# Optimization experiments

Hardware: AMD Instinct MI355X
Metric: run time of the kernel (lower is better)

Reference implementation:

```python
import jax, jax.numpy as jnp
import numpy as np

S, B, D, H = 2048, 64, 128, 128


def setup_inputs() -> dict:
    key = jax.random.key(0)
    ks = jax.random.split(key, 7)
    scale = 1.0 / np.sqrt(H)
    return {
        "input": jax.random.normal(ks[0], (S, B, D), dtype=jnp.float32),
        "time": jax.random.uniform(ks[1], (S, B, 1), dtype=jnp.float32),
        "W_ih": jax.random.normal(ks[2], (4 * H, D), dtype=jnp.float32) * scale,
        "W_hh": jax.random.normal(ks[3], (4 * H, H), dtype=jnp.float32) * scale,
        "b": jax.random.normal(ks[4], (4 * H,), dtype=jnp.float32) * scale,
        "w_t": jax.random.uniform(ks[5], (H,), dtype=jnp.float32),
        "b_t": jax.random.uniform(ks[6], (H,), dtype=jnp.float32),
    }


def reference(input, time, W_ih, W_hh, b, w_t, b_t):
    # ReverseLSTMLayer: run a time-conditioned LSTM cell over REVERSED time steps,
    # then re-reverse the stacked outputs. state starts at zeros (state=None).
    Bsz = input.shape[1]
    Hd = W_hh.shape[1]

    def step(state, xt):
        x, t = xt  # x: [B, D], t: [B, 1]
        h, c = state
        gates = x @ W_ih.T + h @ W_hh.T + b  # [B, 4H]
        i_, f_, g_, o_ = jnp.split(gates, 4, axis=-1)
        i_ = jax.nn.sigmoid(i_)
        f_ = jax.nn.sigmoid(f_)
        g_ = jnp.tanh(g_)
        o_ = jax.nn.sigmoid(o_)
        # learned exponential time decay on the carried cell state (T-LSTM style)
        decay = jnp.exp(-jax.nn.relu(t * w_t + b_t))  # [B, H]
        c = f_ * c * decay + i_ * g_
        h = o_ * jnp.tanh(c)
        return (h, c), h

    init = (jnp.zeros((Bsz, Hd), input.dtype), jnp.zeros((Bsz, Hd), input.dtype))
    # iterate over reversed sequence, then reverse outputs back
    (h, c), ys_rev = jax.lax.scan(step, init, (input[::-1], time[::-1]))
    outputs = ys_rev[::-1]  # [S, B, H]
    return outputs, (h, c)
```

## Files before the change

kernel.cpp:

```cpp
#include <hip/hip_runtime.h>

#define S_LEN 2048
#define B_SZ  64
#define D_IN  128
#define H_SZ  128
#define G4    512

typedef __attribute__((ext_vector_type(4))) float     floatx4;
typedef __attribute__((ext_vector_type(2))) float     floatx2;
typedef __attribute__((ext_vector_type(8))) _Float16  half8;
typedef __attribute__((ext_vector_type(2))) _Float16  half2_t;

template<int CTRL>
__device__ __forceinline__ float qperm(float v) {
  return __int_as_float(
      __builtin_amdgcn_mov_dpp(__float_as_int(v), CTRL, 0xF, 0xF, true));
}

template<int P>
__device__ __forceinline__ half2_t h2ext(half8 v) {
  return __builtin_shufflevector(v, v, 2 * P, 2 * P + 1);
}

__device__ __forceinline__ void lds_barrier() {
  asm volatile("s_waitcnt lgkmcnt(0)\n\ts_barrier" ::: "memory");
}

__global__ __launch_bounds__(256) void gx_gemm(
    const float* __restrict__ X,
    const float* __restrict__ Wih,
    const float* __restrict__ bias,
    _Float16* __restrict__ gx)
{
  __shared__ _Float16 Wl[128][136];
  const int tid  = threadIdx.x;
  const int lane = tid & 63;
  const int wv   = tid >> 6;
  const int R0   = blockIdx.x * 256;
  const int m    = lane & 15;
  const int q    = lane >> 4;

  const float LOG2E = 1.4426950408889634f;

  half8 afrag[4][4];
  #pragma unroll
  for (int rg = 0; rg < 4; ++rg) {
    const float* xrow = X + (size_t)(R0 + rg * 64 + wv * 16 + m) * D_IN;
    #pragma unroll
    for (int kf = 0; kf < 4; ++kf) {
      const int k0 = kf * 32 + q * 8;
      floatx4 v0 = *(const floatx4*)(xrow + k0);
      floatx4 v1 = *(const floatx4*)(xrow + k0 + 4);
      half8 a;
      a[0] = (_Float16)v0.x; a[1] = (_Float16)v0.y;
      a[2] = (_Float16)v0.z; a[3] = (_Float16)v0.w;
      a[4] = (_Float16)v1.x; a[5] = (_Float16)v1.y;
      a[6] = (_Float16)v1.z; a[7] = (_Float16)v1.w;
      afrag[rg][kf] = a;
    }
  }

  for (int nc = 0; nc < 4; ++nc) {
    const float sc = (nc == 2) ? (-2.0f * LOG2E) : (-LOG2E);
    __syncthreads();
    for (int i = tid; i < 128 * 32; i += 256) {
      const int row = i >> 5;
      const int c4  = (i & 31) * 4;
      floatx4 v = *(const floatx4*)(Wih + ((size_t)nc * 128 + row) * D_IN + c4);
      Wl[row][c4 + 0] = (_Float16)v.x;
      Wl[row][c4 + 1] = (_Float16)v.y;
      Wl[row][c4 + 2] = (_Float16)v.z;
      Wl[row][c4 + 3] = (_Float16)v.w;
    }
    __syncthreads();

    #pragma unroll
    for (int nt = 0; nt < 8; ++nt) {
      const int n0  = nc * 128 + nt * 16;
      const int nlo = nt * 16 + m;
      const float bv = bias[n0 + m];
      half8 bfrag[4];
      #pragma unroll
      for (int kf = 0; kf < 4; ++kf)
        bfrag[kf] = *(const half8*)(&Wl[nlo][kf * 32 + q * 8]);
      #pragma unroll
      for (int rg = 0; rg < 4; ++rg) {
        floatx4 acc = {bv, bv, bv, bv};
        #pragma unroll
        for (int kf = 0; kf < 4; ++kf)
          acc = __builtin_amdgcn_mfma_f32_16x16x32_f16(afrag[rg][kf],
                                                       bfrag[kf], acc, 0, 0, 0);
        _Float16* gp =
            gx + (size_t)(R0 + rg * 64 + wv * 16 + q * 4) * G4 + n0 + m;
        #pragma unroll
        for (int r = 0; r < 4; ++r)
          gp[(size_t)r * G4] = (_Float16)(acc[r] * sc);
      }
    }
  }
}

__device__ __forceinline__ float fd(half2_t a, half2_t b, float c) {
  return __builtin_amdgcn_fdot2(a, b, c, false);
}

__device__ __forceinline__ half8 wcvt(const float* __restrict__ p, float sc) {
  floatx4 v0 = *(const floatx4*)p;
  floatx4 v1 = *(const floatx4*)(p + 4);
  half8 h;
  h[0] = (_Float16)(v0.x * sc); h[1] = (_Float16)(v0.y * sc);
  h[2] = (_Float16)(v0.z * sc); h[3] = (_Float16)(v0.w * sc);
  h[4] = (_Float16)(v1.x * sc); h[5] = (_Float16)(v1.y * sc);
  h[6] = (_Float16)(v1.z * sc); h[7] = (_Float16)(v1.w * sc);
  return h;
}

#define PIN_WEIGHTS()                                                         \
  asm volatile(""                                                             \
               : "+v"(w00), "+v"(w01), "+v"(w02), "+v"(w03),                  \
                 "+v"(w10), "+v"(w11), "+v"(w12), "+v"(w13),                  \
                 "+v"(w20), "+v"(w21), "+v"(w22), "+v"(w23),                  \
                 "+v"(w30), "+v"(w31), "+v"(w32), "+v"(w33),                  \
                 "+v"(wt), "+v"(bt))

#define DOT8(HV, WA, WB, WC, WD)                                              \
  {                                                                           \
    q0a = fd(h2ext<0>(HV), h2ext<0>(WA), q0a);                                \
    q1a = fd(h2ext<0>(HV), h2ext<0>(WB), q1a);                                \
    q2a = fd(h2ext<0>(HV), h2ext<0>(WC), q2a);                                \
    q3a = fd(h2ext<0>(HV), h2ext<0>(WD), q3a);                                \
    q0a = fd(h2ext<1>(HV), h2ext<1>(WA), q0a);                                \
    q1a = fd(h2ext<1>(HV), h2ext<1>(WB), q1a);                                \
    q2a = fd(h2ext<1>(HV), h2ext<1>(WC), q2a);                                \
    q3a = fd(h2ext<1>(HV), h2ext<1>(WD), q3a);                                \
    q0b = fd(h2ext<2>(HV), h2ext<2>(WA), q0b);                                \
    q1b = fd(h2ext<2>(HV), h2ext<2>(WB), q1b);                                \
    q2b = fd(h2ext<2>(HV), h2ext<2>(WC), q2b);                                \
    q3b = fd(h2ext<2>(HV), h2ext<2>(WD), q3b);                                \
    q0b = fd(h2ext<3>(HV), h2ext<3>(WA), q0b);                                \
    q1b = fd(h2ext<3>(HV), h2ext<3>(WB), q1b);                                \
    q2b = fd(h2ext<3>(HV), h2ext<3>(WC), q2b);                                \
    q3b = fd(h2ext<3>(HV), h2ext<3>(WD), q3b);                                \
  }

#define GATE(HR, GXV, TMV, CVAR, HVAR)                                        \
  {                                                                           \
    half8 hv0 = *(const half8*)((HR) + 0 * 32 + tt * 8);                      \
    half8 hv1 = *(const half8*)((HR) + 1 * 32 + tt * 8);                      \
    half8 hv2 = *(const half8*)((HR) + 2 * 32 + tt * 8);                      \
    half8 hv3 = *(const half8*)((HR) + 3 * 32 + tt * 8);                      \
    float q0a = 0.f, q0b = 0.f, q1a = 0.f, q1b = 0.f;                         \
    float q2a = 0.f, q2b = 0.f, q3a = 0.f, q3b = 0.f;                         \
    DOT8(hv0, w00, w10, w20, w30);                                            \
    DOT8(hv1, w01, w11, w21, w31);                                            \
    DOT8(hv2, w02, w12, w22, w32);                                            \
    DOT8(hv3, w03, w13, w23, w33);                                            \
    float a0 = q0a + q0b, a1 = q1a + q1b, a2 = q2a + q2b, a3 = q3a + q3b;     \
    a0 += qperm<0xB1>(a0); a1 += qperm<0xB1>(a1);                             \
    a2 += qperm<0xB1>(a2); a3 += qperm<0xB1>(a3);                             \
    a0 += qperm<0x4E>(a0); a1 += qperm<0x4E>(a1);                             \
    a2 += qperm<0x4E>(a2); a3 += qperm<0x4E>(a3);                             \
    float pre = (tt & 1) ? ((tt & 2) ? a3 : a1) : ((tt & 2) ? a2 : a0);       \
    pre += (GXV);            \
    const float e  = __builtin_amdgcn_exp2f(pre);                             \
    const float v  = fmaf(am, __builtin_amdgcn_rcpf(1.0f + e), aa);           \
    float z = fmaf((TMV), wt, bt);                  \
    z = fminf(z, 0.0f);                                   \
    const float d  = __builtin_amdgcn_exp2f(z);                               \
    const float p2 = qperm<0x4E>(v);                                          \
    const float fv = (tt == 1) ? v : p2;                                      \
    const float r  = odd ? fv * (d * (CVAR)) : v * p2;                        \
    const float cn = r + qperm<0xB1>(r);                                      \
    (CVAR) = cn;                                                              \
    const float e2 = __builtin_amdgcn_exp2f(-2.0f * LOG2E * cn);              \
    const float th = fmaf(2.0f, __builtin_amdgcn_rcpf(1.0f + e2), -1.0f);     \
    (HVAR) = v * th;                                                          \
  }

__global__ __launch_bounds__(512)
__attribute__((amdgpu_waves_per_eu(2, 2)))
void lstm_rev(
    const _Float16* __restrict__ gx,
    const float* __restrict__ timep,
    const float* __restrict__ Whh,
    const float* __restrict__ w_tp,
    const float* __restrict__ b_tp,
    float* __restrict__ out)
{
  __shared__ __align__(16) _Float16 hbuf[2][H_SZ];
  const int tid = threadIdx.x;
  const int b   = blockIdx.x;
  const int tt  = tid & 3;
  const int col = tid >> 2;
  const int j   = tt * 128 + col;

  const float LOG2E = 1.4426950408889634f;

  half8 w00, w01, w02, w03, w10, w11, w12, w13;
  half8 w20, w21, w22, w23, w30, w31, w32, w33;
  {
    const float s1 = -LOG2E, s2 = -2.0f * LOG2E;
    const float* r0 = Whh + (size_t)(0 * 128 + col) * H_SZ + tt * 8;
    const float* r1 = Whh + (size_t)(1 * 128 + col) * H_SZ + tt * 8;
    const float* r2 = Whh + (size_t)(2 * 128 + col) * H_SZ + tt * 8;
    const float* r3 = Whh + (size_t)(3 * 128 + col) * H_SZ + tt * 8;
    w00 = wcvt(r0 +  0, s1); w01 = wcvt(r0 + 32, s1);
    w02 = wcvt(r0 + 64, s1); w03 = wcvt(r0 + 96, s1);
    w10 = wcvt(r1 +  0, s1); w11 = wcvt(r1 + 32, s1);
    w12 = wcvt(r1 + 64, s1); w13 = wcvt(r1 + 96, s1);
    w20 = wcvt(r2 +  0, s2); w21 = wcvt(r2 + 32, s2);
    w22 = wcvt(r2 + 64, s2); w23 = wcvt(r2 + 96, s2);
    w30 = wcvt(r3 +  0, s1); w31 = wcvt(r3 + 32, s1);
    w32 = wcvt(r3 + 64, s1); w33 = wcvt(r3 + 96, s1);
  }

  float wt = -LOG2E * w_tp[col];
  float bt = -LOG2E * b_tp[col];
  const float am  = (tt == 2) ? 2.0f : 1.0f;
  const float aa  = (tt == 2) ? -1.0f : 0.0f;
  const bool  odd = (tt & 1) != 0;

  if (tid < 2 * H_SZ) ((_Float16*)hbuf)[tid] = (_Float16)0.0f;
  __syncthreads();

  const size_t go = (size_t)b * G4 + j;

  _Float16 r0 = gx[((size_t)(S_LEN - 1) << 15) + go];
  _Float16 r1 = gx[((size_t)(S_LEN - 2) << 15) + go];
  float tm0 = timep[((S_LEN - 1) << 6) + b];
  float tm1 = timep[((S_LEN - 2) << 6) + b];

  float c = 0.0f;

  for (int t = S_LEN - 1; t > 0; t -= 2) {
    PIN_WEIGHTS();
    {
      const int tl = (t >= 2) ? (t - 2) : 0;
      _Float16 r2 = gx[((size_t)tl << 15) + go];
      float   tm2 = timep[(tl << 6) + b];
      const float g0 = (float)r0;
      float h0;
      GATE(&hbuf[0][0], g0, tm0, c, h0);
      if (tt == 3) {
        hbuf[1][col] = (_Float16)h0;
        out[((size_t)t << 13) + (size_t)b * H_SZ + col] = h0;
      }
      lds_barrier();
      r0 = r1; r1 = r2; tm0 = tm1; tm1 = tm2;
    }
    PIN_WEIGHTS();
    {
      const int T  = t - 1;
      const int tl = (T >= 2) ? (T - 2) : 0;
      _Float16 r2 = gx[((size_t)tl << 15) + go];
      float   tm2 = timep[(tl << 6) + b];
      const float g0 = (float)r0;
      float h0;
      GATE(&hbuf[1][0], g0, tm0, c, h0);
      if (tt == 3) {
        hbuf[0][col] = (_Float16)h0;
        out[((size_t)T << 13) + (size_t)b * H_SZ + col] = h0;
        if (T == 0) {
          float* hf = out + (size_t)S_LEN * B_SZ * H_SZ;
          hf[(size_t)b * H_SZ + col] = h0;
          hf[(size_t)B_SZ * H_SZ + (size_t)b * H_SZ + col] = c;
        }
      }
      lds_barrier();
      r0 = r1; r1 = r2; tm0 = tm1; tm1 = tm2;
    }
  }
}

extern "C" void kernel_launch(void* const* d_in, const int* in_sizes, int n_in,
                              void* d_out, int out_size, void* d_ws, size_t ws_size,
                              hipStream_t stream) {
  const float* input = (const float*)d_in[0];
  const float* timep = (const float*)d_in[1];
  const float* W_ih  = (const float*)d_in[2];
  const float* W_hh  = (const float*)d_in[3];
  const float* bias  = (const float*)d_in[4];
  const float* w_t   = (const float*)d_in[5];
  const float* b_t   = (const float*)d_in[6];
  float* out = (float*)d_out;

  _Float16* gx = (_Float16*)d_ws;

  gx_gemm<<<dim3((S_LEN * B_SZ) / 256), dim3(256), 0, stream>>>(
      input, W_ih, bias, gx);

  lstm_rev<<<dim3(B_SZ), dim3(512), 0, stream>>>(
      gx, timep, W_hh, w_t, b_t, out);
}
```

Measured before the change: 1.375 ms.

## Transpose gx to time-contiguous layout, vector-load gates, stage time in LDS

The projection GEMM now writes gx as [batch][gate][time], so each recurrent thread reads 8 consecutive timesteps with one 16-byte load instead of one scalar fp16 load per step. The time inputs for the whole sequence are preloaded into shared memory once per block, and the recurrent loop is unrolled 8 steps per iteration with prefetch two blocks ahead. This removes per-step global load latency from the serial critical path. In exchange, the GEMM's stores become strided across time, and the kernel uses more LDS and registers.

```diff
diff --git a/kernel.cpp b/kernel.cpp
--- a/kernel.cpp
+++ b/kernel.cpp
@@ -9,6 +9,7 @@
 typedef __attribute__((ext_vector_type(4))) float     floatx4;
 typedef __attribute__((ext_vector_type(2))) float     floatx2;
 typedef __attribute__((ext_vector_type(8))) _Float16  half8;
+typedef __attribute__((ext_vector_type(4))) _Float16  half4;
 typedef __attribute__((ext_vector_type(2))) _Float16  half2_t;
 
 template<int CTRL>
@@ -36,7 +37,8 @@
   const int tid  = threadIdx.x;
   const int lane = tid & 63;
   const int wv   = tid >> 6;
-  const int R0   = blockIdx.x * 256;
+  const int b    = blockIdx.y;
+  const int T0   = blockIdx.x * 256;
   const int m    = lane & 15;
   const int q    = lane >> 4;
 
@@ -45,7 +47,8 @@
   half8 afrag[4][4];
   #pragma unroll
   for (int rg = 0; rg < 4; ++rg) {
-    const float* xrow = X + (size_t)(R0 + rg * 64 + wv * 16 + m) * D_IN;
+    const int t = T0 + rg * 64 + wv * 16 + m;
+    const float* xrow = X + ((size_t)t * B_SZ + b) * D_IN;
     #pragma unroll
     for (int kf = 0; kf < 4; ++kf) {
       const int k0 = kf * 32 + q * 8;
@@ -90,11 +93,13 @@
         for (int kf = 0; kf < 4; ++kf)
           acc = __builtin_amdgcn_mfma_f32_16x16x32_f16(afrag[rg][kf],
                                                        bfrag[kf], acc, 0, 0, 0);
-        _Float16* gp =
-            gx + (size_t)(R0 + rg * 64 + wv * 16 + q * 4) * G4 + n0 + m;
-        #pragma unroll
-        for (int r = 0; r < 4; ++r)
-          gp[(size_t)r * G4] = (_Float16)(acc[r] * sc);
+        const int tbase = T0 + rg * 64 + wv * 16 + q * 4;
+        half4 hv;
+        hv[0] = (_Float16)(acc[0] * sc);
+        hv[1] = (_Float16)(acc[1] * sc);
+        hv[2] = (_Float16)(acc[2] * sc);
+        hv[3] = (_Float16)(acc[3] * sc);
+        *(half4*)(gx + ((size_t)b * G4 + n0 + m) * S_LEN + tbase) = hv;
       }
     }
   }
@@ -177,6 +182,24 @@
     (HVAR) = v * th;                                                          \
   }
 
+#define SUB(K, TMV, RP, WP)                                                   \
+  {                                                                           \
+    const float g0 = (float)cur8[K];                                          \
+    float h0;                                                                 \
+    GATE(&hbuf[RP][0], g0, (TMV), c, h0);                                     \
+    if (tt == 3) {                                                            \
+      hbuf[WP][col] = (_Float16)h0;                                           \
+      const int tcur = blk * 8 + K;                                           \
+      out[((size_t)tcur << 13) + bH + col] = h0;                              \
+      if (tcur == 0) {                                                        \
+        float* hf = out + (size_t)S_LEN * B_SZ * H_SZ;                        \
+        hf[bH + col] = h0;                                                    \
+        hf[(size_t)B_SZ * H_SZ + bH + col] = c;                               \
+      }                                                                       \
+    }                                                                         \
+    lds_barrier();                                                            \
+  }
+
 __global__ __launch_bounds__(512)
 __attribute__((amdgpu_waves_per_eu(2, 2)))
 void lstm_rev(
@@ -188,6 +211,7 @@
     float* __restrict__ out)
 {
   __shared__ __align__(16) _Float16 hbuf[2][H_SZ];
+  __shared__ __align__(16) float    tml[S_LEN];
   const int tid = threadIdx.x;
   const int b   = blockIdx.x;
   const int tt  = tid & 3;
@@ -195,6 +219,12 @@
   const int j   = tt * 128 + col;
 
   const float LOG2E = 1.4426950408889634f;
+
+  #pragma unroll
+  for (int k = 0; k < 4; ++k) {
+    const int idx = tid + k * 512;
+    tml[idx] = timep[(idx << 6) + b];
+  }
 
   half8 w00, w01, w02, w03, w10, w11, w12, w13;
   half8 w20, w21, w22, w23, w30, w31, w32, w33;
@@ -223,52 +253,32 @@
   if (tid < 2 * H_SZ) ((_Float16*)hbuf)[tid] = (_Float16)0.0f;
   __syncthreads();
 
-  const size_t go = (size_t)b * G4 + j;
-
-  _Float16 r0 = gx[((size_t)(S_LEN - 1) << 15) + go];
-  _Float16 r1 = gx[((size_t)(S_LEN - 2) << 15) + go];
-  float tm0 = timep[((S_LEN - 1) << 6) + b];
-  float tm1 = timep[((S_LEN - 2) << 6) + b];
+  const _Float16* gxr = gx + ((size_t)b * G4 + j) * S_LEN;
+  const size_t bH = (size_t)b * H_SZ;
+
+  half8 cur8 = *(const half8*)(gxr + 255 * 8);
+  half8 nxt8 = *(const half8*)(gxr + 254 * 8);
 
   float c = 0.0f;
 
-  for (int t = S_LEN - 1; t > 0; t -= 2) {
+  for (int blk = 255; blk >= 0; --blk) {
     PIN_WEIGHTS();
-    {
-      const int tl = (t >= 2) ? (t - 2) : 0;
-      _Float16 r2 = gx[((size_t)tl << 15) + go];
-      float   tm2 = timep[(tl << 6) + b];
-      const float g0 = (float)r0;
-      float h0;
-      GATE(&hbuf[0][0], g0, tm0, c, h0);
-      if (tt == 3) {
-        hbuf[1][col] = (_Float16)h0;
-        out[((size_t)t << 13) + (size_t)b * H_SZ + col] = h0;
-      }
-      lds_barrier();
-      r0 = r1; r1 = r2; tm0 = tm1; tm1 = tm2;
-    }
-    PIN_WEIGHTS();
-    {
-      const int T  = t - 1;
-      const int tl = (T >= 2) ? (T - 2) : 0;
-      _Float16 r2 = gx[((size_t)tl << 15) + go];
-      float   tm2 = timep[(tl << 6) + b];
-      const float g0 = (float)r0;
-      float h0;
-      GATE(&hbuf[1][0], g0, tm0, c, h0);
-      if (tt == 3) {
-        hbuf[0][col] = (_Float16)h0;
-        out[((size_t)T << 13) + (size_t)b * H_SZ + col] = h0;
-        if (T == 0) {
-          float* hf = out + (size_t)S_LEN * B_SZ * H_SZ;
-          hf[(size_t)b * H_SZ + col] = h0;
-          hf[(size_t)B_SZ * H_SZ + (size_t)b * H_SZ + col] = c;
-        }
-      }
-      lds_barrier();
-      r0 = r1; r1 = r2; tm0 = tm1; tm1 = tm2;
-    }
+    const int pfb = (blk >= 2) ? blk - 2 : 0;
+    half8 fut8 = *(const half8*)(gxr + pfb * 8);
+    const floatx4 tmA = *(const floatx4*)(&tml[blk * 8 + 4]);
+    const floatx4 tmB = *(const floatx4*)(&tml[blk * 8 + 0]);
+
+    SUB(7, tmA.w, 0, 1)
+    SUB(6, tmA.z, 1, 0)
+    SUB(5, tmA.y, 0, 1)
+    SUB(4, tmA.x, 1, 0)
+    SUB(3, tmB.w, 0, 1)
+    SUB(2, tmB.z, 1, 0)
+    SUB(1, tmB.y, 0, 1)
+    SUB(0, tmB.x, 1, 0)
+
+    cur8 = nxt8;
+    nxt8 = fut8;
   }
 }
 
@@ -286,7 +296,7 @@
 
   _Float16* gx = (_Float16*)d_ws;
 
-  gx_gemm<<<dim3((S_LEN * B_SZ) / 256), dim3(256), 0, stream>>>(
+  gx_gemm<<<dim3(S_LEN / 256, B_SZ), dim3(256), 0, stream>>>(
       input, W_ih, bias, gx);
 
   lstm_rev<<<dim3(B_SZ), dim3(512), 0, stream>>>(
```

Measured after the change: 1.287 ms. 6.5% less time.
